# Kernel optimization log

Measured on AMD Instinct MI355X. Metric: run time of the kernel, lower is better.

The kernel has to match this reference:

```python
import jax, jax.numpy as jnp
import numpy as np

B, T, C, U = 256, 512, 256, 64  # batch, time, classes (incl. blank), label length
BLANK = C - 1                   # keras ctc_batch_cost: blank is last class
S = 2 * U + 1                   # extended label length (blanks interleaved)
NEG = -1e30                     # safe log-zero for fp32
EPS = 1e-7                      # keras.backend.epsilon()


def setup_inputs() -> dict:
    key = jax.random.key(0)
    k1, k2 = jax.random.split(key)
    # y_pred are softmax probabilities over time, as fed to ctc_batch_cost
    y_pred = jax.nn.softmax(jax.random.normal(k1, (B, T, C), dtype=jnp.float32), axis=-1)
    # labels exclude the blank index (values in [0, C-2]); all U positions valid
    y_true = jax.random.randint(k2, (B, U), 0, C - 1, dtype=jnp.int32)
    return {"y_true": y_true, "y_pred": y_pred}


def _ctc_loss(y_pred, y_true):
    # keras ctc_batch_cost computes loss on log(y_pred + eps)
    log_probs = jnp.log(y_pred + EPS)                      # [B, T, C]
    # extended label sequence: blank, l1, blank, l2, ..., blank
    ext = jnp.full((B, S), BLANK, dtype=y_true.dtype).at[:, 1::2].set(y_true)
    # gather per-state emission log-probs: lp_ext[b,t,s] = log_probs[b,t,ext[b,s]]
    lp_ext = jnp.take_along_axis(log_probs, ext[:, None, :].astype(jnp.int32), axis=2)  # [B,T,S]
    # skip transition (s-2 -> s) allowed iff ext[s] != blank and ext[s] != ext[s-2]
    ext_m2 = jnp.pad(ext[:, :-2], ((0, 0), (2, 0)), constant_values=-1)
    skip_ok = (ext != BLANK) & (ext != ext_m2)             # [B, S]

    # alpha_0: can start in state 0 (blank) or state 1 (first label)
    alpha0 = (jnp.full((B, S), NEG, dtype=jnp.float32)
              .at[:, 0].set(lp_ext[:, 0, 0])
              .at[:, 1].set(lp_ext[:, 0, 1]))

    def step(alpha, lp_t):
        a1 = jnp.pad(alpha[:, :-1], ((0, 0), (1, 0)), constant_values=NEG)
        a2 = jnp.pad(alpha[:, :-2], ((0, 0), (2, 0)), constant_values=NEG)
        a2 = jnp.where(skip_ok, a2, NEG)
        alpha = jnp.logaddexp(jnp.logaddexp(alpha, a1), a2) + lp_t
        return alpha, None

    lp_time_major = jnp.swapaxes(lp_ext, 0, 1)             # [T, B, S]
    alpha, _ = jax.lax.scan(step, alpha0, lp_time_major[1:])
    # terminate in last blank or last label
    loss = -jnp.logaddexp(alpha[:, -1], alpha[:, -2])      # [B]
    return loss[:, None]                                   # [B, 1] like ctc_batch_cost


def reference(y_true, y_pred):
    return _ctc_loss(y_pred, y_true)
```

## Files before the change

### kernel.cpp

```cpp
#include <hip/hip_runtime.h>


constexpr int B = 256, T = 512, C = 256, U = 64;
constexpr int CH = 16;
constexpr int STR = 68;
#define EPSF 1e-7f

__device__ __forceinline__ float dpp_wave_shr1(float x) {
    return __int_as_float(__builtin_amdgcn_update_dpp(
        0, __float_as_int(x), 0x138, 0xf, 0xf, true));
}

#define DPPMAX(ctrl)                                                      \
    {                                                                     \
        float x_ = __int_as_float(__builtin_amdgcn_update_dpp(            \
            0, __float_as_int(m_), (ctrl), 0xf, 0xf, true));              \
        m_ = fmaxf(m_, x_);                                               \
    }

#define RESCALE()                                                         \
    {                                                                     \
        float m_ = fmaxf(fmaxf(a_even, a_odd), a_top);                    \
        DPPMAX(0x111) DPPMAX(0x112) DPPMAX(0x114) DPPMAX(0x118)           \
        DPPMAX(0x142) DPPMAX(0x143)                                       \
        const float mx_ = __int_as_float(                                 \
            __builtin_amdgcn_readlane(__float_as_int(m_), 63));           \
        int e_ = (__float_as_int(mx_) >> 23) & 0xff;                      \
        int k_ = 187 - e_;                                                \
        k_ = k_ > 127 ? 127 : k_;                                         \
        const float s_ = __int_as_float((k_ + 127) << 23);                \
        a_even *= s_; a_odd *= s_; a_top *= s_;                           \
        esum += k_;                                                       \
    }

#define LOAD_CHUNK(LA, BL, cidx, LP, BP, STRIDE)                          \
    {                                                                     \
        const int c_ = (cidx);                                            \
        _Pragma("unroll")                                                 \
        for (int i = 0; i < CH; ++i) {                                    \
            int t = c_ * CH + i;                                          \
            t = t < T ? t : T - 1;                                        \
            LA[i] = LP[(size_t)t * STRIDE];                               \
            BL[i] = BP[(size_t)t * STRIDE];                               \
        }                                                                 \
    }

#define COMP_CHUNK(LA, BL, cidx)                                          \
    {                                                                     \
        const int c_ = (cidx);                                            \
        _Pragma("unroll")                                                 \
        for (int i = 0; i < CH; ++i) {                                    \
            const int t = c_ * CH + i;                                    \
            const float pb = BL[i] + EPSF;                                \
            const float pl = LA[i] + EPSF;                                \
            const float po = dpp_wave_shr1(a_odd);                        \
            const float skp = skip_ok ? po : 0.f;                         \
            const float ne = (a_even + po) * pb;                          \
            const float no = (a_even + a_odd + skp) * pl;                 \
            const float nt = (a_top + a_odd) * pb;                        \
            a_even = ne; a_odd = no; a_top = nt;                          \
            if ((t & 7) == 7) RESCALE();                                  \
        }                                                                 \
    }

__global__ __launch_bounds__(256) void gather_kernel(const int* __restrict__ y_true,
                                                     const float* __restrict__ y_pred,
                                                     float* __restrict__ compact) {
    __shared__ float buf[4][2][C];
    const int lane = threadIdx.x & 63;
    const int w = threadIdx.x >> 6;
    const int g = blockIdx.x;
    const int b = g >> 3;
    const int r0 = (g & 7) * 64 + w;
    const int lab = y_true[b * U + lane];
    const float* __restrict__ rp = y_pred + (size_t)b * T * C;
    float* __restrict__ cp = compact + (size_t)b * T * STR;

    float4 v = ((const float4*)(rp + (size_t)r0 * C))[lane];
#pragma unroll
    for (int i = 0; i < 16; ++i) {
        const int r = r0 + 4 * i;
        float4 vn = v;
        if (i < 15) vn = ((const float4*)(rp + (size_t)(r + 4) * C))[lane];
        float* bb = &buf[w][i & 1][0];
        ((float4*)bb)[lane] = v;
        const float sel = bb[lab];
        cp[(size_t)r * STR + lane] = sel;
        if (lane == 0) cp[(size_t)r * STR + 64] = bb[C - 1];
        v = vn;
    }
}

template <int STRIDE, bool COMPACT>
__global__ __launch_bounds__(64) void chain_kernel(const int* __restrict__ y_true,
                                                   const float* __restrict__ src,
                                                   float* __restrict__ out) {
    const int b = blockIdx.x;
    const int lane = threadIdx.x;
    const int label = y_true[b * U + lane];
    const int label_prev = __shfl_up(label, 1);
    const bool skip_ok = (lane > 0) && (label != label_prev);
    const float* __restrict__ base = src + (size_t)b * T * STRIDE;
    const float* __restrict__ labp = COMPACT ? (base + lane) : (base + label);
    const float* __restrict__ blkp = COMPACT ? (base + 64) : (base + (C - 1));

    float a_even = (lane == 0) ? 1.f : 0.f, a_odd = 0.f, a_top = 0.f;
    int esum = 0;

    float la0[CH], bl0[CH], la1[CH], bl1[CH];
    LOAD_CHUNK(la0, bl0, 0, labp, blkp, STRIDE);

    for (int c2 = 0; c2 < 16; ++c2) {
        const int c = 2 * c2;
        LOAD_CHUNK(la1, bl1, c + 1, labp, blkp, STRIDE);
        __builtin_amdgcn_sched_barrier(0);
        COMP_CHUNK(la0, bl0, c);
        if (c2 < 15) LOAD_CHUNK(la0, bl0, c + 2, labp, blkp, STRIDE);
        __builtin_amdgcn_sched_barrier(0);
        COMP_CHUNK(la1, bl1, c + 1);
    }

    if (lane == 63)
        out[b] = -logf(a_top + a_odd) + (float)esum * 0.69314718055994531f;
}

extern "C" void kernel_launch(void* const* d_in, const int* in_sizes, int n_in,
                              void* d_out, int out_size, void* d_ws, size_t ws_size,
                              hipStream_t stream) {
    const int* y_true   = (const int*)d_in[0];
    const float* y_pred = (const float*)d_in[1];
    float* out = (float*)d_out;
    const size_t need = (size_t)B * T * STR * sizeof(float);
    if (ws_size >= need) {
        float* compact = (float*)d_ws;
        hipLaunchKernelGGL(gather_kernel, dim3(2048), dim3(256), 0, stream,
                           y_true, y_pred, compact);
        hipLaunchKernelGGL((chain_kernel<STR, true>), dim3(B), dim3(64), 0, stream,
                           y_true, compact, out);
    } else {
        hipLaunchKernelGGL((chain_kernel<C, false>), dim3(B), dim3(64), 0, stream,
                           y_true, y_pred, out);
    }
}
```

Before: 225.7 us.

## Split gather output into label and blank arrays, broadcast blank via readlane

The gather kernel now writes label probabilities into a dense 64-wide array and blank probabilities into a separate per-time array, both with epsilon already added. Each wave handles 32 consecutive rows with a deeper prefetch. The chain kernel loads one blank value per lane per 32-step chunk and broadcasts it with readlane, instead of every lane loading the blank for every step. Chunk size doubles to 32, which cuts redundant loads and moves the epsilon adds out of the serial loop, at the cost of more registers.

```diff
diff --git a/kernel.cpp b/kernel.cpp
--- a/kernel.cpp
+++ b/kernel.cpp
@@ -2,8 +2,7 @@
 
 
 constexpr int B = 256, T = 512, C = 256, U = 64;
-constexpr int CH = 16;
-constexpr int STR = 68;
+constexpr int CH = 32;
 #define EPSF 1e-7f
 
 __device__ __forceinline__ float dpp_wave_shr1(float x) {
@@ -33,24 +32,115 @@
         esum += k_;                                                       \
     }
 
-#define LOAD_CHUNK(LA, BL, cidx, LP, BP, STRIDE)                          \
-    {                                                                     \
-        const int c_ = (cidx);                                            \
+__global__ __launch_bounds__(256) void gather_kernel(const int* __restrict__ y_true,
+                                                     const float* __restrict__ y_pred,
+                                                     float* __restrict__ lab,
+                                                     float* __restrict__ blk) {
+    __shared__ float buf[4][2][C];
+    const int lane = threadIdx.x & 63;
+    const int w = threadIdx.x >> 6;
+    const int g = blockIdx.x;
+    const int b = g >> 2;
+    const int r0 = (g & 3) * 128 + w * 32;
+    const int lb = y_true[b * U + lane];
+    const float4* __restrict__ rp4 =
+        (const float4*)(y_pred + (size_t)b * T * C) + lane;
+    float* __restrict__ lp = lab + (size_t)b * T * 64;
+    float* __restrict__ bp = blk + (size_t)b * T;
+
+    float4 vA  = rp4[(size_t)r0 * 64];
+    float4 vA2 = rp4[(size_t)(r0 + 1) * 64];
+    ((float4*)&buf[w][0][0])[lane] = vA;
+    vA = vA2;
+    vA2 = rp4[(size_t)(r0 + 2) * 64];
+#pragma unroll
+    for (int i = 0; i < 32; ++i) {
+        float4 vB;
+        if (i + 3 < 32) vB = rp4[(size_t)(r0 + i + 3) * 64];
+        const int r = r0 + i;
+        const float* bb = &buf[w][i & 1][0];
+        lp[(size_t)r * 64 + lane] = bb[lb] + EPSF;
+        if (lane == 0) bp[r] = bb[C - 1] + EPSF;
+        if (i + 1 < 32) ((float4*)&buf[w][(i + 1) & 1][0])[lane] = vA;
+        vA = vA2; vA2 = vB;
+    }
+}
+
+#define COMP32(LA, BV, cidx)                                              \
+    {                                                                     \
         _Pragma("unroll")                                                 \
         for (int i = 0; i < CH; ++i) {                                    \
-            int t = c_ * CH + i;                                          \
+            const float pb = __int_as_float(                              \
+                __builtin_amdgcn_readlane(__float_as_int(BV), i));        \
+            const float pl = LA[i];                                       \
+            const float po = dpp_wave_shr1(a_odd);                        \
+            const float skp = skip_ok ? po : 0.f;                         \
+            const float ne = (a_even + po) * pb;                          \
+            const float no = (a_even + a_odd + skp) * pl;                 \
+            const float nt = (a_top + a_odd) * pb;                        \
+            a_even = ne; a_odd = no; a_top = nt;                          \
+            if ((i & 7) == 7) RESCALE();                                  \
+        }                                                                 \
+    }
+
+__global__ __launch_bounds__(64) void chain_compact(const int* __restrict__ y_true,
+                                                    const float* __restrict__ lab,
+                                                    const float* __restrict__ blk,
+                                                    float* __restrict__ out) {
+    const int b = blockIdx.x;
+    const int lane = threadIdx.x;
+    const int label = y_true[b * U + lane];
+    const int label_prev = __shfl_up(label, 1);
+    const bool skip_ok = (lane > 0) && (label != label_prev);
+    const float* __restrict__ labp = lab + (size_t)b * T * 64 + lane;
+    const float* __restrict__ bp = blk + (size_t)b * T;
+
+    float la0[CH], la1[CH];
+    float bv0, bv1;
+#pragma unroll
+    for (int i = 0; i < CH; ++i) la0[i] = labp[(size_t)i * 64];
+    bv0 = bp[lane & 31];
+
+    float a_even = (lane == 0) ? 1.f : 0.f, a_odd = 0.f, a_top = 0.f;
+    int esum = 0;
+
+    for (int c2 = 0; c2 < 8; ++c2) {
+        const int c = 2 * c2;
+#pragma unroll
+        for (int i = 0; i < CH; ++i)
+            la1[i] = labp[((size_t)(c + 1) * CH + i) * 64];
+        bv1 = bp[(c + 1) * CH + (lane & 31)];
+        __builtin_amdgcn_sched_barrier(0);
+        COMP32(la0, bv0, c);
+        if (c2 < 7) {
+#pragma unroll
+            for (int i = 0; i < CH; ++i)
+                la0[i] = labp[((size_t)(c + 2) * CH + i) * 64];
+            bv0 = bp[(c + 2) * CH + (lane & 31)];
+        }
+        __builtin_amdgcn_sched_barrier(0);
+        COMP32(la1, bv1, c + 1);
+    }
+
+    if (lane == 63)
+        out[b] = -logf(a_top + a_odd) + (float)esum * 0.69314718055994531f;
+}
+
+#define LOAD_CHUNK16(LA, BL, cidx)                                        \
+    {                                                                     \
+        _Pragma("unroll")                                                 \
+        for (int i = 0; i < 16; ++i) {                                    \
+            int t = (cidx) * 16 + i;                                      \
             t = t < T ? t : T - 1;                                        \
-            LA[i] = LP[(size_t)t * STRIDE];                               \
-            BL[i] = BP[(size_t)t * STRIDE];                               \
+            LA[i] = labp[(size_t)t * C];                                  \
+            BL[i] = blkp[(size_t)t * C];                                  \
         }                                                                 \
     }
-
-#define COMP_CHUNK(LA, BL, cidx)                                          \
-    {                                                                     \
-        const int c_ = (cidx);                                            \
+#define COMP_CHUNK16(LA, BL, cidx)                                        \
+    {                                                                     \
         _Pragma("unroll")                                                 \
-        for (int i = 0; i < CH; ++i) {                                    \
-            const int t = c_ * CH + i;                                    \
+        for (int i = 0; i < 16; ++i) {                                    \
+            const int t = (cidx) * 16 + i;                                \
             const float pb = BL[i] + EPSF;                                \
             const float pl = LA[i] + EPSF;                                \
             const float po = dpp_wave_shr1(a_odd);                        \
@@ -63,63 +153,31 @@
         }                                                                 \
     }
 
-__global__ __launch_bounds__(256) void gather_kernel(const int* __restrict__ y_true,
-                                                     const float* __restrict__ y_pred,
-                                                     float* __restrict__ compact) {
-    __shared__ float buf[4][2][C];
-    const int lane = threadIdx.x & 63;
-    const int w = threadIdx.x >> 6;
-    const int g = blockIdx.x;
-    const int b = g >> 3;
-    const int r0 = (g & 7) * 64 + w;
-    const int lab = y_true[b * U + lane];
-    const float* __restrict__ rp = y_pred + (size_t)b * T * C;
-    float* __restrict__ cp = compact + (size_t)b * T * STR;
-
-    float4 v = ((const float4*)(rp + (size_t)r0 * C))[lane];
-#pragma unroll
-    for (int i = 0; i < 16; ++i) {
-        const int r = r0 + 4 * i;
-        float4 vn = v;
-        if (i < 15) vn = ((const float4*)(rp + (size_t)(r + 4) * C))[lane];
-        float* bb = &buf[w][i & 1][0];
-        ((float4*)bb)[lane] = v;
-        const float sel = bb[lab];
-        cp[(size_t)r * STR + lane] = sel;
-        if (lane == 0) cp[(size_t)r * STR + 64] = bb[C - 1];
-        v = vn;
-    }
-}
-
-template <int STRIDE, bool COMPACT>
-__global__ __launch_bounds__(64) void chain_kernel(const int* __restrict__ y_true,
-                                                   const float* __restrict__ src,
+__global__ __launch_bounds__(64) void chain_direct(const int* __restrict__ y_true,
+                                                   const float* __restrict__ y_pred,
                                                    float* __restrict__ out) {
     const int b = blockIdx.x;
     const int lane = threadIdx.x;
     const int label = y_true[b * U + lane];
     const int label_prev = __shfl_up(label, 1);
     const bool skip_ok = (lane > 0) && (label != label_prev);
-    const float* __restrict__ base = src + (size_t)b * T * STRIDE;
-    const float* __restrict__ labp = COMPACT ? (base + lane) : (base + label);
-    const float* __restrict__ blkp = COMPACT ? (base + 64) : (base + (C - 1));
+    const float* __restrict__ base = y_pred + (size_t)b * T * C;
+    const float* __restrict__ labp = base + label;
+    const float* __restrict__ blkp = base + (C - 1);
 
     float a_even = (lane == 0) ? 1.f : 0.f, a_odd = 0.f, a_top = 0.f;
     int esum = 0;
-
-    float la0[CH], bl0[CH], la1[CH], bl1[CH];
-    LOAD_CHUNK(la0, bl0, 0, labp, blkp, STRIDE);
-
+    float la0[16], bl0[16], la1[16], bl1[16];
+    LOAD_CHUNK16(la0, bl0, 0);
     for (int c2 = 0; c2 < 16; ++c2) {
         const int c = 2 * c2;
-        LOAD_CHUNK(la1, bl1, c + 1, labp, blkp, STRIDE);
-        __builtin_amdgcn_sched_barrier(0);
-        COMP_CHUNK(la0, bl0, c);
-        if (c2 < 15) LOAD_CHUNK(la0, bl0, c + 2, labp, blkp, STRIDE);
-        __builtin_amdgcn_sched_barrier(0);
-        COMP_CHUNK(la1, bl1, c + 1);
-    }
-
+        LOAD_CHUNK16(la1, bl1, c + 1);
+        __builtin_amdgcn_sched_barrier(0);
+        COMP_CHUNK16(la0, bl0, c);
+        if (c2 < 15) LOAD_CHUNK16(la0, bl0, c + 2);
+        __builtin_amdgcn_sched_barrier(0);
+        COMP_CHUNK16(la1, bl1, c + 1);
+    }
     if (lane == 63)
         out[b] = -logf(a_top + a_odd) + (float)esum * 0.69314718055994531f;
 }
@@ -130,15 +188,17 @@
     const int* y_true   = (const int*)d_in[0];
     const float* y_pred = (const float*)d_in[1];
     float* out = (float*)d_out;
-    const size_t need = (size_t)B * T * STR * sizeof(float);
+    const size_t lab_elems = (size_t)B * T * 64;
+    const size_t need = (lab_elems + (size_t)B * T) * sizeof(float);
     if (ws_size >= need) {
-        float* compact = (float*)d_ws;
-        hipLaunchKernelGGL(gather_kernel, dim3(2048), dim3(256), 0, stream,
-                           y_true, y_pred, compact);
-        hipLaunchKernelGGL((chain_kernel<STR, true>), dim3(B), dim3(64), 0, stream,
-                           y_true, compact, out);
+        float* lab = (float*)d_ws;
+        float* blk = lab + lab_elems;
+        hipLaunchKernelGGL(gather_kernel, dim3(1024), dim3(256), 0, stream,
+                           y_true, y_pred, lab, blk);
+        hipLaunchKernelGGL(chain_compact, dim3(B), dim3(64), 0, stream,
+                           y_true, lab, blk, out);
     } else {
-        hipLaunchKernelGGL((chain_kernel<C, false>), dim3(B), dim3(64), 0, stream,
+        hipLaunchKernelGGL(chain_direct, dim3(B), dim3(64), 0, stream,
                            y_true, y_pred, out);
     }
 }
```

Result: faster. 210.7 us (-6.7%).
